# Performance work log

Measured on AMD Instinct MI355X. Metric: run time of the kernel, lower is better.

## Reference

```python
import jax, jax.numpy as jnp
import numpy as np

L, B, F, E, H, V, NL, K = 32, 128, 4096, 512, 512, 50000, 2, 20


def setup_inputs() -> dict:
    key = jax.random.key(0)
    ks = jax.random.split(key, 9)
    return {
        "dialog_encoder_inputs": jax.random.randint(ks[0], (L, B), 0, V),
        "fact_inputs": jax.random.normal(ks[1], (B, F, E), dtype=jnp.float32),
        "h": jax.random.normal(ks[2], (NL, B, H), dtype=jnp.float32),
        "c": jax.random.normal(ks[3], (NL, B, H), dtype=jnp.float32),
        "enc_emb": jax.random.normal(ks[4], (V, E), dtype=jnp.float32) * 0.02,
        "Aw": jax.random.normal(ks[5], (H, E), dtype=jnp.float32) * 0.04,
        "Ab": jnp.zeros((H,), dtype=jnp.float32),
        "Cw": jax.random.normal(ks[6], (H, E), dtype=jnp.float32) * 0.04,
        "Cb": jnp.zeros((H,), dtype=jnp.float32),
        "top_k": K,
    }


def reference(dialog_encoder_inputs, fact_inputs, h, c, enc_emb, Aw, Ab, Cw, Cb, top_k):
    # --- get_top_k_fact_average: embed dialog, score facts, gather top-k ---
    q = enc_emb[dialog_encoder_inputs].mean(axis=0)                # [B, E] mean-pooled query
    scores = jnp.einsum('be,bfe->bf', q, fact_inputs)              # [B, F] similarity
    _, idx = jax.lax.top_k(scores, top_k)                          # [B, K]
    topf = jnp.take_along_axis(fact_inputs, idx[:, :, None], axis=1)  # [B, K, E]

    # --- facts_forward: memory-network style hidden-state update ---
    fact_M = jnp.einsum('bke,he->bkh', topf, Aw) + Ab              # fact_linearA
    fact_C = jnp.einsum('bke,he->bkh', topf, Cw) + Cb              # fact_linearC

    def update(u):  # u: [NL, B, H]
        P = jax.nn.softmax(jnp.einsum('bke,lbe->lbk', topf, u), axis=-1)  # attn over facts
        o = jnp.einsum('lbk,bke->lbe', P, topf)                           # weighted fact avg
        return o + u

    return update(h), update(c), fact_M, fact_C
```

## Files before the change

kernel.cpp:

```cpp
#include <hip/hip_runtime.h>
#include <float.h>
#include <math.h>

#define LL 32
#define BB 128
#define FF 4096
#define EE 512
#define HH 512
#define NLAYER 2
#define KK 20

typedef float f4 __attribute__((ext_vector_type(4)));
typedef short bf16x8 __attribute__((ext_vector_type(8)));
typedef float f32x4 __attribute__((ext_vector_type(4)));

__device__ inline unsigned short bf16rne(float x) {
    unsigned u = __float_as_uint(x);
    u += 0x7fff + ((u >> 16) & 1);
    return (unsigned short)(u >> 16);
}

__global__ __launch_bounds__(256) void q_kernel(const int* __restrict__ tok,
                                                const float* __restrict__ emb,
                                                float* __restrict__ q) {
    int b = blockIdx.x, eh = blockIdx.y;
    __shared__ int ts[LL];
    if (threadIdx.x < LL) ts[threadIdx.x] = tok[threadIdx.x * BB + b];
    __syncthreads();
    int e = eh * 256 + threadIdx.x;
    float acc = 0.f;
    #pragma unroll
    for (int l = 0; l < LL; ++l) acc += emb[(long)ts[l] * EE + e];
    q[b * EE + e] = acc * (1.0f / LL);
}

__global__ __launch_bounds__(256) void convw_kernel(const float* __restrict__ Aw,
                                                    const float* __restrict__ Cw,
                                                    unsigned short* __restrict__ Wbf) {
    const float* W = blockIdx.y ? Cw : Aw;
    unsigned short* dst = Wbf + (size_t)blockIdx.y * HH * EE;
    int i = (blockIdx.x * 256 + threadIdx.x) * 4;
    float4 v = *(const float4*)(W + i);
    ushort4 o;
    o.x = bf16rne(v.x); o.y = bf16rne(v.y); o.z = bf16rne(v.z); o.w = bf16rne(v.w);
    *(ushort4*)(dst + i) = o;
}

__global__ __launch_bounds__(256) void scores_kernel(const float* __restrict__ q,
                                                     const float* __restrict__ fact,
                                                     float* __restrict__ scores) {
    int b = blockIdx.y;
    int wave = threadIdx.x >> 6;
    int lane = threadIdx.x & 63;
    const f4* qv = (const f4*)(q + b * EE);
    f4 qa = qv[lane];
    f4 qb = qv[64 + lane];
    int f0 = (blockIdx.x * 4 + wave) * 8;
    #pragma unroll
    for (int i = 0; i < 8; ++i) {
        int f = f0 + i;
        const f4* fv = (const f4*)(fact + ((long)b * FF + f) * EE);
        f4 fa = __builtin_nontemporal_load(fv + lane);
        f4 fb = __builtin_nontemporal_load(fv + 64 + lane);
        f4 p = qa * fa + qb * fb;
        float d = p.x + p.y + p.z + p.w;
        #pragma unroll
        for (int off = 32; off > 0; off >>= 1) d += __shfl_xor(d, off, 64);
        if (lane == 0) scores[b * FF + f] = d;
    }
}

__global__ __launch_bounds__(256) void topk_update_kernel(const float* __restrict__ scores,
                                                          const float* __restrict__ fact,
                                                          const float* __restrict__ hin,
                                                          const float* __restrict__ cin,
                                                          unsigned short* __restrict__ topfb,
                                                          float* __restrict__ out) {
    int b = blockIdx.x;
    __shared__ float vals[FF];
    __shared__ float tf[KK][EE];
    __shared__ unsigned long long wbest[4];
    __shared__ int sel[KK];
    int t = threadIdx.x;
    int wave = t >> 6, lane = t & 63;

    const float4* sv = (const float4*)(scores + b * FF);
    float4* vv = (float4*)vals;
    for (int i = t; i < FF / 4; i += 256) vv[i] = sv[i];
    __syncthreads();

    for (int it = 0; it < KK; ++it) {
        unsigned long long best = 0;
        #pragma unroll
        for (int s = 0; s < FF / 256; ++s) {
            int j = t + s * 256;
            unsigned u = __float_as_uint(vals[j]);
            u ^= ((int)u >> 31) | 0x80000000u;
            unsigned long long key = ((unsigned long long)u << 32) | (unsigned)(FF - 1 - j);
            if (key > best) best = key;
        }
        #pragma unroll
        for (int off = 32; off > 0; off >>= 1) {
            unsigned hi = (unsigned)(best >> 32), lo = (unsigned)best;
            unsigned ohi = __shfl_xor(hi, off, 64);
            unsigned olo = __shfl_xor(lo, off, 64);
            unsigned long long o = ((unsigned long long)ohi << 32) | olo;
            if (o > best) best = o;
        }
        if (lane == 0) wbest[wave] = best;
        __syncthreads();
        if (t == 0) {
            unsigned long long bb = wbest[0];
            if (wbest[1] > bb) bb = wbest[1];
            if (wbest[2] > bb) bb = wbest[2];
            if (wbest[3] > bb) bb = wbest[3];
            int idx = FF - 1 - (int)(bb & 0xFFFFFFFFu);
            sel[it] = idx;
            vals[idx] = -FLT_MAX;
        }
        __syncthreads();
    }

    for (int kk = 0; kk < KK; kk += 2) {
        int k = kk + (t >> 7);
        int e = t & 127;
        int src = sel[k];
        float4 v = *(const float4*)(fact + (((long)b * FF + src) * EE) + e * 4);
        *(float4*)&tf[k][e * 4] = v;
        ushort4 o;
        o.x = bf16rne(v.x); o.y = bf16rne(v.y); o.z = bf16rne(v.z); o.w = bf16rne(v.w);
        *(ushort4*)(topfb + ((size_t)b * KK + k) * EE + e * 4) = o;
    }
    __syncthreads();

    const float* u = (wave < 2 ? hin : cin) + ((size_t)(wave & 1) * BB + b) * EE;
    const float4* uv = (const float4*)u;
    float4 ua = uv[lane], ub = uv[64 + lane];
    float sk[KK];
    #pragma unroll
    for (int k = 0; k < KK; ++k) {
        const float4* tv = (const float4*)&tf[k][0];
        float4 ta = tv[lane], tb = tv[64 + lane];
        float d = ua.x * ta.x + ua.y * ta.y + ua.z * ta.z + ua.w * ta.w
                + ub.x * tb.x + ub.y * tb.y + ub.z * tb.z + ub.w * tb.w;
        #pragma unroll
        for (int off = 32; off > 0; off >>= 1) d += __shfl_xor(d, off, 64);
        sk[k] = d;
    }
    float m = sk[0];
    #pragma unroll
    for (int k = 1; k < KK; ++k) m = fmaxf(m, sk[k]);
    float sum = 0.f;
    #pragma unroll
    for (int k = 0; k < KK; ++k) { sk[k] = __expf(sk[k] - m); sum += sk[k]; }
    float inv = 1.f / sum;
    float4 oa = {0, 0, 0, 0}, ob = {0, 0, 0, 0};
    #pragma unroll
    for (int k = 0; k < KK; ++k) {
        float p = sk[k] * inv;
        const float4* tv = (const float4*)&tf[k][0];
        float4 ta = tv[lane], tb = tv[64 + lane];
        oa.x += p * ta.x; oa.y += p * ta.y; oa.z += p * ta.z; oa.w += p * ta.w;
        ob.x += p * tb.x; ob.y += p * tb.y; ob.z += p * tb.z; ob.w += p * tb.w;
    }
    oa.x += ua.x; oa.y += ua.y; oa.z += ua.z; oa.w += ua.w;
    ob.x += ub.x; ob.y += ub.y; ob.z += ub.z; ob.w += ub.w;
    float* obase = out + (size_t)(wave < 2 ? 0 : NLAYER * BB * HH)
                       + ((size_t)(wave & 1) * BB + b) * HH;
    float4* ov = (float4*)obase;
    ov[lane] = oa;
    ov[64 + lane] = ob;
}

__global__ __launch_bounds__(256) void factmc_kernel(const unsigned short* __restrict__ topfb,
                                                     const unsigned short* __restrict__ Wbf,
                                                     const float* __restrict__ Ab,
                                                     const float* __restrict__ Cb,
                                                     float* __restrict__ out) {
    int b = blockIdx.x, mat = blockIdx.y;
    const unsigned short* W = Wbf + (size_t)mat * HH * EE;
    const float* bias = mat ? Cb : Ab;
    float* O = out + (size_t)2 * NLAYER * BB * HH
                   + (size_t)mat * BB * KK * HH + (size_t)b * KK * HH;

    __shared__ unsigned short tf[32 * EE];
    {
        const unsigned short* src = topfb + (size_t)b * KK * EE;
        for (int ib = threadIdx.x; ib < KK * EE / 8; ib += 256) {
            int row = ib >> 6;
            int cb = ib & 63;
            float4 v = *(const float4*)(src + row * EE + cb * 8);
            int byte = (row * 1024 + cb * 16) ^ ((row & 7) << 4);
            *(float4*)((char*)tf + byte) = v;
        }
    }
    __syncthreads();

    int wave = threadIdx.x >> 6, lane = threadIdx.x & 63;
    int lrow = lane & 15, lk = lane >> 4;
    f32x4 acc[2][8];
    #pragma unroll
    for (int m = 0; m < 2; ++m)
        #pragma unroll
        for (int n = 0; n < 8; ++n) acc[m][n] = (f32x4){0, 0, 0, 0};

    int h0 = wave * 128 + lrow;
    const unsigned short* wbase = W + (size_t)h0 * EE + lk * 8;

    #pragma unroll 2
    for (int ks = 0; ks < 16; ++ks) {
        int col2 = (ks * 32 + lk * 8) * 2;
        int byte0 = (lrow * 1024 + col2) ^ ((lrow & 7) << 4);
        bf16x8 a0 = *(const bf16x8*)((const char*)tf + byte0);
        int r1 = 16 + lrow;
        int byte1 = (r1 * 1024 + col2) ^ ((r1 & 7) << 4);
        bf16x8 a1 = *(const bf16x8*)((const char*)tf + byte1);
        #pragma unroll
        for (int n = 0; n < 8; ++n) {
            bf16x8 bfrag = *(const bf16x8*)(wbase + (size_t)n * 16 * EE + ks * 32);
            acc[0][n] = __builtin_amdgcn_mfma_f32_16x16x32_bf16(a0, bfrag, acc[0][n], 0, 0, 0);
            acc[1][n] = __builtin_amdgcn_mfma_f32_16x16x32_bf16(a1, bfrag, acc[1][n], 0, 0, 0);
        }
    }

    #pragma unroll
    for (int n = 0; n < 8; ++n) {
        int h = wave * 128 + n * 16 + lrow;
        float bv = bias[h];
        #pragma unroll
        for (int r = 0; r < 4; ++r) {
            int k0 = lk * 4 + r;
            O[(size_t)k0 * HH + h] = acc[0][n][r] + bv;
            int k1 = 16 + lk * 4 + r;
            if (k1 < KK) O[(size_t)k1 * HH + h] = acc[1][n][r] + bv;
        }
    }
}

extern "C" void kernel_launch(void* const* d_in, const int* in_sizes, int n_in,
                              void* d_out, int out_size, void* d_ws, size_t ws_size,
                              hipStream_t stream) {
    const int* tok = (const int*)d_in[0];
    const float* fact = (const float*)d_in[1];
    const float* hin = (const float*)d_in[2];
    const float* cin = (const float*)d_in[3];
    const float* emb = (const float*)d_in[4];
    const float* Aw = (const float*)d_in[5];
    const float* Ab = (const float*)d_in[6];
    const float* Cw = (const float*)d_in[7];
    const float* Cb = (const float*)d_in[8];
    float* out = (float*)d_out;

    float* ws = (float*)d_ws;
    float* q = ws;
    float* scores = ws + 65536;
    unsigned short* topfb = (unsigned short*)(ws + 65536 + 524288);
    unsigned short* Wbf = (unsigned short*)(ws + 65536 + 524288 + 655360);

    q_kernel<<<dim3(BB, 2), 256, 0, stream>>>(tok, emb, q);
    convw_kernel<<<dim3(HH * EE / 1024, 2), 256, 0, stream>>>(Aw, Cw, Wbf);
    scores_kernel<<<dim3(FF / 32, BB), 256, 0, stream>>>(q, fact, scores);
    topk_update_kernel<<<BB, 256, 0, stream>>>(scores, fact, hin, cin, topfb, out);
    factmc_kernel<<<dim3(BB, 2), 256, 0, stream>>>(topfb, Wbf, Ab, Cb, out);
}
```

Measured before the change: 222.6 us.

## Fuse prep kernels and top-k/update/fact-linear into fewer launches

Merges the query-embedding and weight-conversion kernels into one launch, and fuses top-k selection, the h/c update and the fact_M/fact_C MFMA matmuls into a single per-batch kernel that keeps the bf16 top-k facts in swizzled shared memory. This removes the global round trip of the bf16 top-k buffer and two kernel launches. The scores kernel also replaces eight separate 6-step wave reductions with a transposed butterfly reduction that gives each group of eight lanes one fact's sum. In exchange the fused kernel runs only 128 blocks with more shared memory and does both matmuls serially, so the matmul phase loses the parallelism of the former 256-block grid.

```diff
diff --git a/kernel.cpp b/kernel.cpp
--- a/kernel.cpp
+++ b/kernel.cpp
@@ -20,30 +20,35 @@
     return (unsigned short)(u >> 16);
 }
 
-__global__ __launch_bounds__(256) void q_kernel(const int* __restrict__ tok,
-                                                const float* __restrict__ emb,
-                                                float* __restrict__ q) {
-    int b = blockIdx.x, eh = blockIdx.y;
-    __shared__ int ts[LL];
-    if (threadIdx.x < LL) ts[threadIdx.x] = tok[threadIdx.x * BB + b];
-    __syncthreads();
-    int e = eh * 256 + threadIdx.x;
-    float acc = 0.f;
-    #pragma unroll
-    for (int l = 0; l < LL; ++l) acc += emb[(long)ts[l] * EE + e];
-    q[b * EE + e] = acc * (1.0f / LL);
-}
-
-__global__ __launch_bounds__(256) void convw_kernel(const float* __restrict__ Aw,
-                                                    const float* __restrict__ Cw,
-                                                    unsigned short* __restrict__ Wbf) {
-    const float* W = blockIdx.y ? Cw : Aw;
-    unsigned short* dst = Wbf + (size_t)blockIdx.y * HH * EE;
-    int i = (blockIdx.x * 256 + threadIdx.x) * 4;
-    float4 v = *(const float4*)(W + i);
-    ushort4 o;
-    o.x = bf16rne(v.x); o.y = bf16rne(v.y); o.z = bf16rne(v.z); o.w = bf16rne(v.w);
-    *(ushort4*)(dst + i) = o;
+__global__ __launch_bounds__(256) void prep_kernel(const int* __restrict__ tok,
+                                                   const float* __restrict__ emb,
+                                                   float* __restrict__ q,
+                                                   const float* __restrict__ Aw,
+                                                   const float* __restrict__ Cw,
+                                                   unsigned short* __restrict__ Wbf) {
+    int bid = blockIdx.x;
+    if (bid < 256) {
+        int b = bid >> 1, eh = bid & 1;
+        __shared__ int ts[LL];
+        if (threadIdx.x < LL) ts[threadIdx.x] = tok[threadIdx.x * BB + b];
+        __syncthreads();
+        int e = eh * 256 + threadIdx.x;
+        float acc = 0.f;
+        #pragma unroll
+        for (int l = 0; l < LL; ++l) acc += emb[(long)ts[l] * EE + e];
+        q[b * EE + e] = acc * (1.0f / LL);
+    } else {
+        int cid = bid - 256;
+        int matY = cid >> 8;
+        int blkX = cid & 255;
+        const float* W = matY ? Cw : Aw;
+        unsigned short* dst = Wbf + (size_t)matY * HH * EE;
+        int i = (blkX * 256 + threadIdx.x) * 4;
+        float4 v = *(const float4*)(W + i);
+        ushort4 o;
+        o.x = bf16rne(v.x); o.y = bf16rne(v.y); o.z = bf16rne(v.z); o.w = bf16rne(v.w);
+        *(ushort4*)(dst + i) = o;
+    }
 }
 
 __global__ __launch_bounds__(256) void scores_kernel(const float* __restrict__ q,
@@ -56,29 +61,59 @@
     f4 qa = qv[lane];
     f4 qb = qv[64 + lane];
     int f0 = (blockIdx.x * 4 + wave) * 8;
+    float d[8];
     #pragma unroll
     for (int i = 0; i < 8; ++i) {
-        int f = f0 + i;
-        const f4* fv = (const f4*)(fact + ((long)b * FF + f) * EE);
+        const f4* fv = (const f4*)(fact + ((long)b * FF + f0 + i) * EE);
         f4 fa = __builtin_nontemporal_load(fv + lane);
         f4 fb = __builtin_nontemporal_load(fv + 64 + lane);
         f4 p = qa * fa + qb * fb;
-        float d = p.x + p.y + p.z + p.w;
-        #pragma unroll
-        for (int off = 32; off > 0; off >>= 1) d += __shfl_xor(d, off, 64);
-        if (lane == 0) scores[b * FF + f] = d;
-    }
-}
-
-__global__ __launch_bounds__(256) void topk_update_kernel(const float* __restrict__ scores,
-                                                          const float* __restrict__ fact,
-                                                          const float* __restrict__ hin,
-                                                          const float* __restrict__ cin,
-                                                          unsigned short* __restrict__ topfb,
-                                                          float* __restrict__ out) {
+        d[i] = p.x + p.y + p.z + p.w;
+    }
+    bool h32 = lane & 32;
+    float e0, e1, e2, e3;
+    {
+        float s0 = __shfl_xor(d[0], 32), s1 = __shfl_xor(d[1], 32);
+        float s2 = __shfl_xor(d[2], 32), s3 = __shfl_xor(d[3], 32);
+        float s4 = __shfl_xor(d[4], 32), s5 = __shfl_xor(d[5], 32);
+        float s6 = __shfl_xor(d[6], 32), s7 = __shfl_xor(d[7], 32);
+        e0 = h32 ? d[4] + s4 : d[0] + s0;
+        e1 = h32 ? d[5] + s5 : d[1] + s1;
+        e2 = h32 ? d[6] + s6 : d[2] + s2;
+        e3 = h32 ? d[7] + s7 : d[3] + s3;
+    }
+    bool h16 = lane & 16;
+    float g0, g1;
+    {
+        float s0 = __shfl_xor(e0, 16), s1 = __shfl_xor(e1, 16);
+        float s2 = __shfl_xor(e2, 16), s3 = __shfl_xor(e3, 16);
+        g0 = h16 ? e2 + s2 : e0 + s0;
+        g1 = h16 ? e3 + s3 : e1 + s1;
+    }
+    bool h8 = lane & 8;
+    float hs;
+    {
+        float s0 = __shfl_xor(g0, 8), s1 = __shfl_xor(g1, 8);
+        hs = h8 ? g1 + s1 : g0 + s0;
+    }
+    hs += __shfl_xor(hs, 4);
+    hs += __shfl_xor(hs, 2);
+    hs += __shfl_xor(hs, 1);
+    if ((lane & 7) == 0) scores[b * FF + f0 + ((lane >> 3) & 7)] = hs;
+}
+
+__global__ __launch_bounds__(256) void fused_kernel(const float* __restrict__ scores,
+                                                    const float* __restrict__ fact,
+                                                    const float* __restrict__ hin,
+                                                    const float* __restrict__ cin,
+                                                    const unsigned short* __restrict__ Wbf,
+                                                    const float* __restrict__ Ab,
+                                                    const float* __restrict__ Cb,
+                                                    float* __restrict__ out) {
     int b = blockIdx.x;
     __shared__ float vals[FF];
     __shared__ float tf[KK][EE];
+    __shared__ unsigned short tfb[32 * EE];
     __shared__ unsigned long long wbest[4];
     __shared__ int sel[KK];
     int t = threadIdx.x;
@@ -87,6 +122,11 @@
     const float4* sv = (const float4*)(scores + b * FF);
     float4* vv = (float4*)vals;
     for (int i = t; i < FF / 4; i += 256) vv[i] = sv[i];
+    {
+        float4 z = {0, 0, 0, 0};
+        for (int i = t; i < 12 * 1024 / 16; i += 256)
+            *(float4*)((char*)tfb + 20 * 1024 + i * 16) = z;
+    }
     __syncthreads();
 
     for (int it = 0; it < KK; ++it) {
@@ -129,110 +169,91 @@
         *(float4*)&tf[k][e * 4] = v;
         ushort4 o;
         o.x = bf16rne(v.x); o.y = bf16rne(v.y); o.z = bf16rne(v.z); o.w = bf16rne(v.w);
-        *(ushort4*)(topfb + ((size_t)b * KK + k) * EE + e * 4) = o;
+        int byte = (k * 1024 + e * 8) ^ ((k & 7) << 4);
+        *(ushort4*)((char*)tfb + byte) = o;
     }
     __syncthreads();
 
-    const float* u = (wave < 2 ? hin : cin) + ((size_t)(wave & 1) * BB + b) * EE;
-    const float4* uv = (const float4*)u;
-    float4 ua = uv[lane], ub = uv[64 + lane];
-    float sk[KK];
-    #pragma unroll
-    for (int k = 0; k < KK; ++k) {
-        const float4* tv = (const float4*)&tf[k][0];
-        float4 ta = tv[lane], tb = tv[64 + lane];
-        float d = ua.x * ta.x + ua.y * ta.y + ua.z * ta.z + ua.w * ta.w
-                + ub.x * tb.x + ub.y * tb.y + ub.z * tb.z + ub.w * tb.w;
-        #pragma unroll
-        for (int off = 32; off > 0; off >>= 1) d += __shfl_xor(d, off, 64);
-        sk[k] = d;
-    }
-    float m = sk[0];
-    #pragma unroll
-    for (int k = 1; k < KK; ++k) m = fmaxf(m, sk[k]);
-    float sum = 0.f;
-    #pragma unroll
-    for (int k = 0; k < KK; ++k) { sk[k] = __expf(sk[k] - m); sum += sk[k]; }
-    float inv = 1.f / sum;
-    float4 oa = {0, 0, 0, 0}, ob = {0, 0, 0, 0};
-    #pragma unroll
-    for (int k = 0; k < KK; ++k) {
-        float p = sk[k] * inv;
-        const float4* tv = (const float4*)&tf[k][0];
-        float4 ta = tv[lane], tb = tv[64 + lane];
-        oa.x += p * ta.x; oa.y += p * ta.y; oa.z += p * ta.z; oa.w += p * ta.w;
-        ob.x += p * tb.x; ob.y += p * tb.y; ob.z += p * tb.z; ob.w += p * tb.w;
-    }
-    oa.x += ua.x; oa.y += ua.y; oa.z += ua.z; oa.w += ua.w;
-    ob.x += ub.x; ob.y += ub.y; ob.z += ub.z; ob.w += ub.w;
-    float* obase = out + (size_t)(wave < 2 ? 0 : NLAYER * BB * HH)
-                       + ((size_t)(wave & 1) * BB + b) * HH;
-    float4* ov = (float4*)obase;
-    ov[lane] = oa;
-    ov[64 + lane] = ob;
-}
-
-__global__ __launch_bounds__(256) void factmc_kernel(const unsigned short* __restrict__ topfb,
-                                                     const unsigned short* __restrict__ Wbf,
-                                                     const float* __restrict__ Ab,
-                                                     const float* __restrict__ Cb,
-                                                     float* __restrict__ out) {
-    int b = blockIdx.x, mat = blockIdx.y;
-    const unsigned short* W = Wbf + (size_t)mat * HH * EE;
-    const float* bias = mat ? Cb : Ab;
-    float* O = out + (size_t)2 * NLAYER * BB * HH
-                   + (size_t)mat * BB * KK * HH + (size_t)b * KK * HH;
-
-    __shared__ unsigned short tf[32 * EE];
-    {
-        const unsigned short* src = topfb + (size_t)b * KK * EE;
-        for (int ib = threadIdx.x; ib < KK * EE / 8; ib += 256) {
-            int row = ib >> 6;
-            int cb = ib & 63;
-            float4 v = *(const float4*)(src + row * EE + cb * 8);
-            int byte = (row * 1024 + cb * 16) ^ ((row & 7) << 4);
-            *(float4*)((char*)tf + byte) = v;
-        }
-    }
-    __syncthreads();
-
-    int wave = threadIdx.x >> 6, lane = threadIdx.x & 63;
-    int lrow = lane & 15, lk = lane >> 4;
-    f32x4 acc[2][8];
-    #pragma unroll
-    for (int m = 0; m < 2; ++m)
-        #pragma unroll
-        for (int n = 0; n < 8; ++n) acc[m][n] = (f32x4){0, 0, 0, 0};
-
-    int h0 = wave * 128 + lrow;
-    const unsigned short* wbase = W + (size_t)h0 * EE + lk * 8;
-
-    #pragma unroll 2
-    for (int ks = 0; ks < 16; ++ks) {
-        int col2 = (ks * 32 + lk * 8) * 2;
-        int byte0 = (lrow * 1024 + col2) ^ ((lrow & 7) << 4);
-        bf16x8 a0 = *(const bf16x8*)((const char*)tf + byte0);
-        int r1 = 16 + lrow;
-        int byte1 = (r1 * 1024 + col2) ^ ((r1 & 7) << 4);
-        bf16x8 a1 = *(const bf16x8*)((const char*)tf + byte1);
-        #pragma unroll
-        for (int n = 0; n < 8; ++n) {
-            bf16x8 bfrag = *(const bf16x8*)(wbase + (size_t)n * 16 * EE + ks * 32);
-            acc[0][n] = __builtin_amdgcn_mfma_f32_16x16x32_bf16(a0, bfrag, acc[0][n], 0, 0, 0);
-            acc[1][n] = __builtin_amdgcn_mfma_f32_16x16x32_bf16(a1, bfrag, acc[1][n], 0, 0, 0);
-        }
-    }
-
-    #pragma unroll
-    for (int n = 0; n < 8; ++n) {
-        int h = wave * 128 + n * 16 + lrow;
-        float bv = bias[h];
-        #pragma unroll
-        for (int r = 0; r < 4; ++r) {
-            int k0 = lk * 4 + r;
-            O[(size_t)k0 * HH + h] = acc[0][n][r] + bv;
-            int k1 = 16 + lk * 4 + r;
-            if (k1 < KK) O[(size_t)k1 * HH + h] = acc[1][n][r] + bv;
+    {
+        const float* u = (wave < 2 ? hin : cin) + ((size_t)(wave & 1) * BB + b) * EE;
+        const float4* uv = (const float4*)u;
+        float4 ua = uv[lane], ub = uv[64 + lane];
+        float sk[KK];
+        #pragma unroll
+        for (int k = 0; k < KK; ++k) {
+            const float4* tv = (const float4*)&tf[k][0];
+            float4 ta = tv[lane], tb = tv[64 + lane];
+            float d = ua.x * ta.x + ua.y * ta.y + ua.z * ta.z + ua.w * ta.w
+                    + ub.x * tb.x + ub.y * tb.y + ub.z * tb.z + ub.w * tb.w;
+            #pragma unroll
+            for (int off = 32; off > 0; off >>= 1) d += __shfl_xor(d, off, 64);
+            sk[k] = d;
+        }
+        float m = sk[0];
+        #pragma unroll
+        for (int k = 1; k < KK; ++k) m = fmaxf(m, sk[k]);
+        float sum = 0.f;
+        #pragma unroll
+        for (int k = 0; k < KK; ++k) { sk[k] = __expf(sk[k] - m); sum += sk[k]; }
+        float inv = 1.f / sum;
+        float4 oa = {0, 0, 0, 0}, ob = {0, 0, 0, 0};
+        #pragma unroll
+        for (int k = 0; k < KK; ++k) {
+            float p = sk[k] * inv;
+            const float4* tv = (const float4*)&tf[k][0];
+            float4 ta = tv[lane], tb = tv[64 + lane];
+            oa.x += p * ta.x; oa.y += p * ta.y; oa.z += p * ta.z; oa.w += p * ta.w;
+            ob.x += p * tb.x; ob.y += p * tb.y; ob.z += p * tb.z; ob.w += p * tb.w;
+        }
+        oa.x += ua.x; oa.y += ua.y; oa.z += ua.z; oa.w += ua.w;
+        ob.x += ub.x; ob.y += ub.y; ob.z += ub.z; ob.w += ub.w;
+        float* obase = out + (size_t)(wave < 2 ? 0 : NLAYER * BB * HH)
+                           + ((size_t)(wave & 1) * BB + b) * HH;
+        float4* ov = (float4*)obase;
+        ov[lane] = oa;
+        ov[64 + lane] = ob;
+    }
+
+    {
+        int lrow = lane & 15, lk = lane >> 4;
+        for (int mat = 0; mat < 2; ++mat) {
+            const unsigned short* W = Wbf + (size_t)mat * HH * EE;
+            const float* bias = mat ? Cb : Ab;
+            float* O = out + (size_t)2 * NLAYER * BB * HH
+                           + (size_t)mat * BB * KK * HH + (size_t)b * KK * HH;
+            f32x4 acc[2][8];
+            #pragma unroll
+            for (int m = 0; m < 2; ++m)
+                #pragma unroll
+                for (int n = 0; n < 8; ++n) acc[m][n] = (f32x4){0, 0, 0, 0};
+            const unsigned short* wbase = W + (size_t)(wave * 128 + lrow) * EE + lk * 8;
+            #pragma unroll 2
+            for (int ks = 0; ks < 16; ++ks) {
+                int col2 = (ks * 32 + lk * 8) * 2;
+                int byte0 = (lrow * 1024 + col2) ^ ((lrow & 7) << 4);
+                bf16x8 a0 = *(const bf16x8*)((const char*)tfb + byte0);
+                int r1 = 16 + lrow;
+                int byte1 = (r1 * 1024 + col2) ^ ((r1 & 7) << 4);
+                bf16x8 a1 = *(const bf16x8*)((const char*)tfb + byte1);
+                #pragma unroll
+                for (int n = 0; n < 8; ++n) {
+                    bf16x8 bfrag = *(const bf16x8*)(wbase + (size_t)n * 16 * EE + ks * 32);
+                    acc[0][n] = __builtin_amdgcn_mfma_f32_16x16x32_bf16(a0, bfrag, acc[0][n], 0, 0, 0);
+                    acc[1][n] = __builtin_amdgcn_mfma_f32_16x16x32_bf16(a1, bfrag, acc[1][n], 0, 0, 0);
+                }
+            }
+            #pragma unroll
+            for (int n = 0; n < 8; ++n) {
+                int h = wave * 128 + n * 16 + lrow;
+                float bv = bias[h];
+                #pragma unroll
+                for (int r = 0; r < 4; ++r) {
+                    int k0 = lk * 4 + r;
+                    O[(size_t)k0 * HH + h] = acc[0][n][r] + bv;
+                    int k1 = 16 + lk * 4 + r;
+                    if (k1 < KK) O[(size_t)k1 * HH + h] = acc[1][n][r] + bv;
+                }
+            }
         }
     }
 }
@@ -254,12 +275,9 @@
     float* ws = (float*)d_ws;
     float* q = ws;
     float* scores = ws + 65536;
-    unsigned short* topfb = (unsigned short*)(ws + 65536 + 524288);
-    unsigned short* Wbf = (unsigned short*)(ws + 65536 + 524288 + 655360);
-
-    q_kernel<<<dim3(BB, 2), 256, 0, stream>>>(tok, emb, q);
-    convw_kernel<<<dim3(HH * EE / 1024, 2), 256, 0, stream>>>(Aw, Cw, Wbf);
+    unsigned short* Wbf = (unsigned short*)(ws + 65536 + 524288);
+
+    prep_kernel<<<768, 256, 0, stream>>>(tok, emb, q, Aw, Cw, Wbf);
     scores_kernel<<<dim3(FF / 32, BB), 256, 0, stream>>>(q, fact, scores);
-    topk_update_kernel<<<BB, 256, 0, stream>>>(scores, fact, hin, cin, topfb, out);
-    factmc_kernel<<<dim3(BB, 2), 256, 0, stream>>>(topfb, Wbf, Ab, Cb, out);
-}
+    fused_kernel<<<BB, 256, 0, stream>>>(scores, fact, hin, cin, Wbf, Ab, Cb, out);
+}
```

Result: slower. 238.5 us (+7.2%).
